# Kernel tuning notes

Measured on AMD Instinct MI355X. Metric: run time of the kernel, lower is better.

The kernel has to match this reference:

```python
import jax, jax.numpy as jnp
import numpy as np

H, W, C = 512, 512, 288  # SAT resolution and channels (ntheta*nphi = 9*32)
N = 131072               # number of query points


def setup_inputs() -> dict:
    key = jax.random.key(0)
    k1, k2 = jax.random.split(key)
    sat = jax.random.normal(k1, (H, W, C), dtype=jnp.float32)
    x = jax.random.uniform(k2, (N, 4), dtype=jnp.float32)  # [cu, cv, du, dv] in [0,1)
    return {"sat": sat, "x": x, "start_idx": -1, "len_idx": 1}


def reference(sat, x, start_idx, len_idx):
    Hh, Ww, Cc = sat.shape
    resf = jnp.array([Hh, Ww], jnp.float32)
    resi = jnp.array([Hh, Ww], jnp.int32)
    duv = jnp.array([1.0 / Hh, 1.0 / Ww], jnp.float32)
    sat_flat = sat.reshape(-1, Cc)
    if start_idx >= 0:
        sat_flat = sat_flat[:, start_idx:start_idx + len_idx]

    def sample(u):  # u: [N, 2] -> [N, Cq]
        idx = jnp.floor(u * resf - 0.5).astype(jnp.int32)
        bad = jnp.any((idx < 0) | (idx >= resi), axis=-1, keepdims=True)
        lin = jnp.clip(idx[:, 0], 0, Hh - 1) * Ww + jnp.clip(idx[:, 1], 0, Ww - 1)
        return jnp.where(bad, 0.0, sat_flat[lin])

    def query(suv, euv):  # inclusive box sum via 4-corner SAT lookup
        r = sample(euv) + sample(suv - duv)
        r = r - sample(jnp.stack([suv[:, 0] - duv[0], euv[:, 1]], -1))
        r = r - sample(jnp.stack([euv[:, 0], suv[:, 1] - duv[1]], -1))
        return r

    cuv = x[:, :2]
    d = x[:, 2:]
    suv = cuv - d / 2
    euv = cuv + d / 2
    # per-axis swap when the footprint extent is negative
    nsuv = jnp.where(d < 0, euv, suv)
    neuv = jnp.where(d < 0, suv, euv)
    # toroidal wraparound into [0, 1)
    nsuv = nsuv - jnp.floor(nsuv)
    neuv = neuv - jnp.floor(neuv)
    sx, sy = nsuv[:, 0], nsuv[:, 1]
    ex, ey = neuv[:, 0], neuv[:, 1]
    n = x.shape[0]
    bru = jnp.full((n,), 1.0 - duv[0] / 2, jnp.float32)
    brv = jnp.full((n,), 1.0 - duv[1] / 2, jnp.float32)
    tlu = 1.0 - bru
    tlv = 1.0 - brv
    st = lambda a, b: jnp.stack([a, b], -1)

    # case 1: no wrap on either axis
    c = ((sx <= ex) & (sy <= ey))[:, None]
    result = jnp.where(c, query(nsuv, neuv), 0.0)
    # case 2: wrap in u only -> two boxes
    c = ((sx > ex) & (sy <= ey))[:, None]
    result += jnp.where(c, query(nsuv, st(bru, ey)), 0.0)
    result += jnp.where(c, query(st(tlu, sy), neuv), 0.0)
    # case 3: wrap in v only -> two boxes
    c = ((sx <= ex) & (sy > ey))[:, None]
    result += jnp.where(c, query(nsuv, st(ex, brv)), 0.0)
    result += jnp.where(c, query(st(sx, tlv), neuv), 0.0)
    # case 4: wrap in both -> four boxes
    c = ((sx > ex) & (sy > ey))[:, None]
    result += jnp.where(c, query(st(tlu, tlv), neuv), 0.0)
    result += jnp.where(c, query(nsuv, st(bru, brv)), 0.0)
    result += jnp.where(c, query(st(sx, tlv), st(bru, ey)), 0.0)
    result += jnp.where(c, query(st(tlu, sy), st(ex, brv)), 0.0)
    return result
```

## Files before the change

### kernel.cpp

```cpp
#include <hip/hip_runtime.h>


constexpr int Hdim = 512;
constexpr int Wdim = 512;
constexpr int Cdim = 288;

typedef float f32x4 __attribute__((ext_vector_type(4)));

__device__ __forceinline__ void axis_prep(float u, float s, int& idx, float& sgn) {
    int i = (int)floorf(u * 512.0f - 0.5f);
    bool ok = (unsigned)i < 512u;
    idx = ok ? i : 0;
    sgn = ok ? s : 0.0f;
}

template <int K>
__device__ __forceinline__ void gather(const float* __restrict__ sat,
                                       const int* off, const float* sgn,
                                       int lane, int widx,
                                       f32x4& a, f32x4& b) {
    f32x4 v[K], w[K];
#pragma unroll
    for (int k = 0; k < K; ++k) {
        int offk = __builtin_amdgcn_readfirstlane(off[k]);
        const f32x4* __restrict__ row = (const f32x4*)(sat + offk);
        v[k] = row[lane];
        w[k] = row[widx];
    }
#pragma unroll
    for (int k = 0; k < K; ++k) {
        float s = sgn[k];
        a += s * v[k];
        b += s * w[k];
    }
}

template <int NU, int NV>
__device__ __forceinline__ void run_case(const float* __restrict__ sat,
                                         const int* iu, const float* fu,
                                         const int* iv, const float* fv,
                                         int lane, int widx,
                                         f32x4& a, f32x4& b) {
    int off[NU * NV];
    float sgn[NU * NV];
#pragma unroll
    for (int i = 0; i < NU; ++i)
#pragma unroll
        for (int j = 0; j < NV; ++j) {
            off[i * NV + j] = (iu[i] * Wdim + iv[j]) * Cdim;
            sgn[i * NV + j] = fu[i] * fv[j];
        }
    gather<NU * NV>(sat, off, sgn, lane, widx, a, b);
}

__global__ __launch_bounds__(256) void sat_query_kernel(
    const float* __restrict__ sat, const float* __restrict__ x,
    float* __restrict__ out, int n) {
    int wave = (int)((blockIdx.x * blockDim.x + threadIdx.x) >> 6);
    int lane = (int)(threadIdx.x & 63);
    if (wave >= n) return;

    float4 xr = ((const float4*)x)[wave];
    float cu = xr.x, cv = xr.y, d0 = xr.z, d1 = xr.w;

    const float du = 1.0f / 512.0f;

    float su = cu - d0 * 0.5f, eu = cu + d0 * 0.5f;
    float sv = cv - d1 * 0.5f, ev = cv + d1 * 0.5f;
    float nsu = (d0 < 0.0f) ? eu : su, neu = (d0 < 0.0f) ? su : eu;
    float nsv = (d1 < 0.0f) ? ev : sv, nev = (d1 < 0.0f) ? sv : ev;
    nsu -= floorf(nsu); neu -= floorf(neu);
    nsv -= floorf(nsv); nev -= floorf(nev);

    bool wx = nsu > neu;
    bool wy = nsv > nev;

    int iu[3]; float fu[3];
    axis_prep(neu,       1.0f, iu[0], fu[0]);
    axis_prep(nsu - du, -1.0f, iu[1], fu[1]);
    iu[2] = Hdim - 1; fu[2] = 1.0f;

    int iv[3]; float fv[3];
    axis_prep(nev,       1.0f, iv[0], fv[0]);
    axis_prep(nsv - du, -1.0f, iv[1], fv[1]);
    iv[2] = Wdim - 1; fv[2] = 1.0f;

    f32x4 acc_a = {0.f, 0.f, 0.f, 0.f};
    f32x4 acc_b = {0.f, 0.f, 0.f, 0.f};
    int widx = (lane & 7) + 64;

    if (!wx && !wy) {
        run_case<2, 2>(sat, iu, fu, iv, fv, lane, widx, acc_a, acc_b);
    } else if (wx && !wy) {
        run_case<3, 2>(sat, iu, fu, iv, fv, lane, widx, acc_a, acc_b);
    } else if (!wx && wy) {
        run_case<2, 3>(sat, iu, fu, iv, fv, lane, widx, acc_a, acc_b);
    } else {
        run_case<3, 3>(sat, iu, fu, iv, fv, lane, widx, acc_a, acc_b);
    }

    f32x4* __restrict__ orow = (f32x4*)(out + (size_t)wave * Cdim);
    __builtin_nontemporal_store(acc_a, orow + lane);
    if (lane < 8) __builtin_nontemporal_store(acc_b, orow + lane + 64);
}

extern "C" void kernel_launch(void* const* d_in, const int* in_sizes, int n_in,
                              void* d_out, int out_size, void* d_ws, size_t ws_size,
                              hipStream_t stream) {
    const float* sat = (const float*)d_in[0];
    const float* x   = (const float*)d_in[1];
    float* out = (float*)d_out;
    int n = in_sizes[1] / 4;

    int rows_per_block = 4;
    int blocks = (n + rows_per_block - 1) / rows_per_block;
    sat_query_kernel<<<dim3(blocks), dim3(256), 0, stream>>>(sat, x, out, n);
}
```

Before: 472.3 us.

## Sort queries by SAT corner bucket via counting sort for gather locality

Adds a counting-sort pre-pass (zero, histogram, scan, scatter kernels) that buckets queries by the end-corner SAT cell, then runs the main gather kernel in that permuted order, writing results back to the original row. The intent is to make concurrently running waves touch nearby SAT rows so the 302 MB table sees better L2/MALL reuse instead of random DRAM reads. It adds four small kernel launches, atomics, and an indirection load, and falls back to the unsorted path when workspace is insufficient.

```diff
diff --git a/kernel.cpp b/kernel.cpp
--- a/kernel.cpp
+++ b/kernel.cpp
@@ -4,8 +4,10 @@
 constexpr int Hdim = 512;
 constexpr int Wdim = 512;
 constexpr int Cdim = 288;
+constexpr int NQB  = 4096;
 
 typedef float f32x4 __attribute__((ext_vector_type(4)));
+
 
 __device__ __forceinline__ void axis_prep(float u, float s, int& idx, float& sgn) {
     int i = (int)floorf(u * 512.0f - 0.5f);
@@ -13,6 +15,69 @@
     idx = ok ? i : 0;
     sgn = ok ? s : 0.0f;
 }
+
+__device__ __forceinline__ int query_key(float cu, float cv, float d0, float d1) {
+    float su = cu - d0 * 0.5f, eu = cu + d0 * 0.5f;
+    float sv = cv - d1 * 0.5f, ev = cv + d1 * 0.5f;
+    float neu = (d0 < 0.0f) ? su : eu;
+    float nev = (d1 < 0.0f) ? sv : ev;
+    neu -= floorf(neu);
+    nev -= floorf(nev);
+    int iu = (int)floorf(neu * 512.0f - 0.5f);
+    int iv = (int)floorf(nev * 512.0f - 0.5f);
+    iu = min(max(iu, 0), 511);
+    iv = min(max(iv, 0), 511);
+    return (iu << 3) | (iv >> 6);
+}
+
+
+__global__ __launch_bounds__(256) void k_zero(int* hist) {
+    int i = blockIdx.x * blockDim.x + threadIdx.x;
+    if (i < 2 * NQB) hist[i] = 0;
+}
+
+__global__ __launch_bounds__(256) void k_hist(const float4* __restrict__ x, int n,
+                                              int* __restrict__ hist) {
+    for (int q = blockIdx.x * blockDim.x + threadIdx.x; q < n;
+         q += gridDim.x * blockDim.x) {
+        float4 xr = x[q];
+        atomicAdd(&hist[query_key(xr.x, xr.y, xr.z, xr.w)], 1);
+    }
+}
+
+__global__ __launch_bounds__(256) void k_scan(const int* __restrict__ hist,
+                                              int* __restrict__ offs) {
+    __shared__ int part[256];
+    int t = threadIdx.x;
+    int base = t * 16;
+    int local[16];
+    int s = 0;
+#pragma unroll
+    for (int i = 0; i < 16; ++i) { local[i] = hist[base + i]; s += local[i]; }
+    part[t] = s;
+    __syncthreads();
+    for (int d = 1; d < 256; d <<= 1) {
+        int v = (t >= d) ? part[t - d] : 0;
+        __syncthreads();
+        part[t] += v;
+        __syncthreads();
+    }
+    int run = part[t] - s;
+#pragma unroll
+    for (int i = 0; i < 16; ++i) { offs[base + i] = run; run += local[i]; }
+}
+
+__global__ __launch_bounds__(256) void k_scatter(const float4* __restrict__ x, int n,
+                                                 int* __restrict__ offs,
+                                                 int* __restrict__ perm) {
+    for (int q = blockIdx.x * blockDim.x + threadIdx.x; q < n;
+         q += gridDim.x * blockDim.x) {
+        float4 xr = x[q];
+        int pos = atomicAdd(&offs[query_key(xr.x, xr.y, xr.z, xr.w)], 1);
+        perm[pos] = q;
+    }
+}
+
 
 template <int K>
 __device__ __forceinline__ void gather(const float* __restrict__ sat,
@@ -55,12 +120,13 @@
 
 __global__ __launch_bounds__(256) void sat_query_kernel(
     const float* __restrict__ sat, const float* __restrict__ x,
-    float* __restrict__ out, int n) {
+    float* __restrict__ out, int n, const int* __restrict__ perm) {
     int wave = (int)((blockIdx.x * blockDim.x + threadIdx.x) >> 6);
     int lane = (int)(threadIdx.x & 63);
     if (wave >= n) return;
+    int qid = perm ? perm[wave] : wave;
 
-    float4 xr = ((const float4*)x)[wave];
+    float4 xr = ((const float4*)x)[qid];
     float cu = xr.x, cv = xr.y, d0 = xr.z, d1 = xr.w;
 
     const float du = 1.0f / 512.0f;
@@ -99,7 +165,7 @@
         run_case<3, 3>(sat, iu, fu, iv, fv, lane, widx, acc_a, acc_b);
     }
 
-    f32x4* __restrict__ orow = (f32x4*)(out + (size_t)wave * Cdim);
+    f32x4* __restrict__ orow = (f32x4*)(out + (size_t)qid * Cdim);
     __builtin_nontemporal_store(acc_a, orow + lane);
     if (lane < 8) __builtin_nontemporal_store(acc_b, orow + lane + 64);
 }
@@ -112,7 +178,20 @@
     float* out = (float*)d_out;
     int n = in_sizes[1] / 4;
 
-    int rows_per_block = 4;
-    int blocks = (n + rows_per_block - 1) / rows_per_block;
-    sat_query_kernel<<<dim3(blocks), dim3(256), 0, stream>>>(sat, x, out, n);
+    int blocks = (n + 3) / 4;
+
+    size_t need = (size_t)(2 * NQB + n) * sizeof(int);
+    if (d_ws != nullptr && ws_size >= need) {
+        int* hist = (int*)d_ws;
+        int* offs = hist + NQB;
+        int* perm = offs + NQB;
+        int gsb = (n + 255) / 256;
+        k_zero<<<dim3((2 * NQB + 255) / 256), dim3(256), 0, stream>>>(hist);
+        k_hist<<<dim3(gsb), dim3(256), 0, stream>>>((const float4*)x, n, hist);
+        k_scan<<<dim3(1), dim3(256), 0, stream>>>(hist, offs);
+        k_scatter<<<dim3(gsb), dim3(256), 0, stream>>>((const float4*)x, n, offs, perm);
+        sat_query_kernel<<<dim3(blocks), dim3(256), 0, stream>>>(sat, x, out, n, perm);
+    } else {
+        sat_query_kernel<<<dim3(blocks), dim3(256), 0, stream>>>(sat, x, out, n, nullptr);
+    }
 }
```

After: 495.1 us. 4.8% more time.
